# Optimization experiments

Hardware: AMD Instinct MI355X
Metric: run time of the kernel (lower is better)

The kernel has to match this reference:

```python
import jax, jax.numpy as jnp
import numpy as np

LEAKY_SLOPE = 0.2

def leaky_relu(x):
    return jnp.where(x >= 0, x, LEAKY_SLOPE * x)

def setup_inputs() -> dict:
    key = jax.random.key(0)
    ks = jax.random.split(key, 11)
    B, F = 512, 1024
    H1, H2, OUT = 512, 256, 128  # hidden_dims = [512, 256, 128]
    KD = 5                        # minibatch kernel dims
    x = jax.random.normal(ks[0], (B, F), dtype=jnp.float32)
    # features: Linear(F,H1) -> LReLU -> Linear(H1,H2) -> LReLU
    W1 = jax.random.normal(ks[1], (F, H1), dtype=jnp.float32) / np.sqrt(F)
    b1 = jnp.zeros((H1,), dtype=jnp.float32)
    W2 = jax.random.normal(ks[2], (H1, H2), dtype=jnp.float32) / np.sqrt(H1)
    b2 = jnp.zeros((H2,), dtype=jnp.float32)
    # minibatch discrimination tensor T: (in=H2, out=OUT, kernel=KD), N(0,1) init
    T = jax.random.normal(ks[3], (H2, OUT, KD), dtype=jnp.float32)
    # final: Linear(H2+OUT, OUT) -> LReLU -> Linear(OUT, 1)
    W3 = jax.random.normal(ks[4], (H2 + OUT, OUT), dtype=jnp.float32) / np.sqrt(H2 + OUT)
    b3 = jnp.zeros((OUT,), dtype=jnp.float32)
    W4 = jax.random.normal(ks[5], (OUT, 1), dtype=jnp.float32) / np.sqrt(OUT)
    b4 = jnp.zeros((1,), dtype=jnp.float32)
    return {"x": x, "W1": W1, "b1": b1, "W2": W2, "b2": b2,
            "T": T, "W3": W3, "b3": b3, "W4": W4, "b4": b4}

def reference(x, W1, b1, W2, b2, T, W3, b3, W4, b4):
    # MLP feature stack (dropout = identity in eval mode)
    h = leaky_relu(x @ W1 + b1)          # (B, 512)
    h = leaky_relu(h @ W2 + b2)          # (B, 256)
    # Minibatch discrimination
    in_f, out_f, kd = T.shape
    M = (h @ T.reshape(in_f, out_f * kd)).reshape(-1, out_f, kd)  # (B, out, kd)
    # pairwise L1 over kernel dim: (B, B, out)
    norm = jnp.abs(M[:, None, :, :] - M[None, :, :, :]).sum(-1)
    o_b = jnp.exp(-norm).sum(0) - 1.0    # (B, out); -1 removes self term
    z = jnp.concatenate([h, o_b], axis=1)  # (B, 256+128)
    z = leaky_relu(z @ W3 + b3)
    return z @ W4 + b4                    # (B, 1)
```

## Files before the change

### kernel.cpp

```cpp
#include <hip/hip_runtime.h>
#include <math.h>

#define B_   512
#define F_   1024
#define H1_  512
#define H2_  256
#define OUT_ 128
#define KD_  5
#define NT_  640
#define ZK_  384

typedef short bf16x8 __attribute__((ext_vector_type(8)));
typedef float f32x16 __attribute__((ext_vector_type(16)));

__device__ __forceinline__ float lrelu(float v) { return v >= 0.f ? v : 0.2f * v; }

__device__ __forceinline__ unsigned f2bf(float f) {
    unsigned u = __float_as_uint(f);
    return (u + 0x7fffu + ((u >> 16) & 1u)) >> 16;
}
__device__ __forceinline__ unsigned pack2bf(float a, float b) {
    return f2bf(a) | (f2bf(b) << 16);
}

#define NXB 256
#define NW1 512
#define NW2 128
#define NTT 160
#define PACK_BLOCKS (NXB + NW1 + NW2 + NTT + 48)

__global__ __launch_bounds__(256)
void pack_kernel(const float* __restrict__ x,  const float* __restrict__ W1,
                 const float* __restrict__ W2, const float* __restrict__ T,
                 const float* __restrict__ W3,
                 unsigned short* __restrict__ xb,  unsigned short* __restrict__ W1t,
                 unsigned short* __restrict__ W2t, unsigned short* __restrict__ Tt,
                 unsigned short* __restrict__ W3t)
{
    int b = blockIdx.x;
    const int t = threadIdx.x;
    if (b < NXB) {
        const int base = b * 2048 + t * 8;
        const float4 a = *(const float4*)(x + base);
        const float4 c = *(const float4*)(x + base + 4);
        uint4 o;
        o.x = pack2bf(a.x, a.y); o.y = pack2bf(a.z, a.w);
        o.z = pack2bf(c.x, c.y); o.w = pack2bf(c.z, c.w);
        *(uint4*)(xb + base) = o;
        return;
    }
    __shared__ float Tl[32][33];
    const float* src; unsigned short* dst; int R, C, tile;
    b -= NXB;
    if (b < NW1)              { src = W1; dst = W1t; R = 1024; C = 512; tile = b; }
    else if ((b -= NW1) < NW2){ src = W2; dst = W2t; R = 512;  C = 256; tile = b; }
    else if ((b -= NW2) < NTT){ src = T;  dst = Tt;  R = 256;  C = 640; tile = b; }
    else                      { b -= NTT;  src = W3; dst = W3t; R = 384; C = 128; tile = b; }
    const int tpc = C / 32;
    const int tr = tile / tpc, tc = tile % tpc;
    {
        const int col = t & 31, rr = t >> 5;
        #pragma unroll
        for (int p = 0; p < 4; ++p)
            Tl[rr + 8 * p][col] = src[(size_t)(tr * 32 + rr + 8 * p) * C + tc * 32 + col];
    }
    __syncthreads();
    const int orow = t >> 3, up = t & 7;
    unsigned* d = (unsigned*)(dst + (size_t)(tc * 32 + orow) * R + tr * 32);
    d[up]     = pack2bf(Tl[2 * up][orow],      Tl[2 * up + 1][orow]);
    d[up + 8] = pack2bf(Tl[2 * up + 16][orow], Tl[2 * up + 17][orow]);
}

template<int WAVES, int KSLICE, int LDA, int LDB,
         bool RELU, bool HAS_BIAS, bool BF16_OUT, bool CONCAT_A>
__global__ __launch_bounds__(WAVES * 64)
void gemm(const unsigned short* __restrict__ Ab,
          const float* __restrict__ obA, const float* __restrict__ obB,
          const unsigned short* __restrict__ Bt,
          const float* __restrict__ bias,
          void* __restrict__ Cout, int M, int N)
{
    __shared__ float Red[WAVES * 1024];
    const int tid  = threadIdx.x;
    const int wav  = tid >> 6;
    const int lane = tid & 63;
    const int half = lane >> 5;
    const int mn   = lane & 31;
    const int m0   = blockIdx.y * 32;
    const int n0   = blockIdx.x * 32;
    const int kw   = wav * KSLICE;

    f32x16 acc;
    #pragma unroll
    for (int i = 0; i < 16; ++i) acc[i] = 0.f;

    const unsigned short* arow = Ab + (size_t)(m0 + mn) * LDA;
    const unsigned short* brow = Bt + (size_t)(n0 + mn) * LDB;

    #pragma unroll
    for (int s = 0; s < KSLICE / 16; ++s) {
        const int k = kw + 16 * s + 8 * half;
        bf16x8 af, bf;
        if (CONCAT_A) {
            if (k < H2_) {
                af = *(const bf16x8*)&Ab[(size_t)(m0 + mn) * H2_ + k];
            } else {
                const float* pa = obA + (size_t)(m0 + mn) * OUT_ + (k - H2_);
                const float* pb = obB + (size_t)(m0 + mn) * OUT_ + (k - H2_);
                union { unsigned u[4]; bf16x8 v; } cv;
                #pragma unroll
                for (int jj = 0; jj < 4; ++jj)
                    cv.u[jj] = pack2bf(pa[2 * jj] + pb[2 * jj],
                                       pa[2 * jj + 1] + pb[2 * jj + 1]);
                af = cv.v;
            }
        } else {
            af = *(const bf16x8*)&arow[k];
        }
        bf = *(const bf16x8*)&brow[k];
        acc = __builtin_amdgcn_mfma_f32_32x32x16_bf16(af, bf, acc, 0, 0, 0);
    }

    #pragma unroll
    for (int r = 0; r < 16; ++r) {
        const int row = (r & 3) + 8 * (r >> 2) + 4 * half;
        Red[wav * 1024 + row * 32 + mn] = acc[r];
    }
    __syncthreads();

    if (tid < 256) {
        const int e0 = tid * 4, row = e0 >> 5, col = e0 & 31;
        float v[4];
        #pragma unroll
        for (int q = 0; q < 4; ++q) {
            float u = 0.f;
            #pragma unroll
            for (int w = 0; w < WAVES; ++w) u += Red[w * 1024 + e0 + q];
            if (HAS_BIAS) u += bias[n0 + col + q];
            if (RELU) u = lrelu(u);
            v[q] = u;
        }
        if (BF16_OUT) {
            uint2 o;
            o.x = pack2bf(v[0], v[1]); o.y = pack2bf(v[2], v[3]);
            *(uint2*)((unsigned short*)Cout + (size_t)(m0 + row) * N + n0 + col) = o;
        } else {
            *(float4*)((float*)Cout + (size_t)(m0 + row) * N + n0 + col) =
                make_float4(v[0], v[1], v[2], v[3]);
        }
    }
}

__global__ __launch_bounds__(128)
void disc_kernel(const float* __restrict__ Mt, float* __restrict__ obH)
{
    const int o  = blockIdx.x >> 3;
    const int jq = (blockIdx.x >> 1) & 3;
    const int ih = blockIdx.x & 1;
    const int t  = threadIdx.x;
    const int j  = jq * 128 + t;
    const int i0 = ih * 256;
    __shared__ float L[256 * 8];
    const float* base = Mt + (size_t)o * 5 * 512;
    #pragma unroll
    for (int k = 0; k < KD_; ++k) {
        L[t * 8 + k]         = base[k * 512 + i0 + t];
        L[(t + 128) * 8 + k] = base[k * 512 + i0 + t + 128];
    }
    const float mj0 = base[0 * 512 + j], mj1 = base[1 * 512 + j],
                mj2 = base[2 * 512 + j], mj3 = base[3 * 512 + j],
                mj4 = base[4 * 512 + j];
    __syncthreads();

    float acc0 = 0.f, acc1 = 0.f;
    #pragma unroll 4
    for (int i = 0; i < 256; i += 2) {
        {
            const float4 a = *(const float4*)&L[i * 8];
            const float n = fabsf(a.x - mj0) + fabsf(a.y - mj1) + fabsf(a.z - mj2)
                          + fabsf(a.w - mj3) + fabsf(L[i * 8 + 4] - mj4);
            acc0 += __expf(-n);
        }
        {
            const float4 a = *(const float4*)&L[(i + 1) * 8];
            const float n = fabsf(a.x - mj0) + fabsf(a.y - mj1) + fabsf(a.z - mj2)
                          + fabsf(a.w - mj3) + fabsf(L[(i + 1) * 8 + 4] - mj4);
            acc1 += __expf(-n);
        }
    }
    const float self = ((j >> 8) == ih) ? 1.f : 0.f;
    obH[(size_t)ih * B_ * OUT_ + (size_t)j * OUT_ + o] = acc0 + acc1 - self;
}

__global__ __launch_bounds__(256)
void final_dot(const float* __restrict__ z3, const float* __restrict__ W4,
               const float* __restrict__ b4, float* __restrict__ out)
{
    const int t = threadIdx.x;
    const int row = blockIdx.x * 64 + (t >> 2);
    const int q = t & 3;
    const float4* z = (const float4*)(z3 + (size_t)row * OUT_ + q * 32);
    const float4* w = (const float4*)(W4 + q * 32);
    float acc = 0.f;
    #pragma unroll
    for (int k = 0; k < 8; ++k) {
        const float4 a = z[k], b = w[k];
        acc += a.x * b.x + a.y * b.y + a.z * b.z + a.w * b.w;
    }
    acc += __shfl_down(acc, 2, 4);
    acc += __shfl_down(acc, 1, 4);
    if (q == 0) out[row] = acc + b4[0];
}

extern "C" void kernel_launch(void* const* d_in, const int* in_sizes, int n_in,
                              void* d_out, int out_size, void* d_ws, size_t ws_size,
                              hipStream_t stream) {
    const float* x  = (const float*)d_in[0];
    const float* W1 = (const float*)d_in[1];
    const float* b1 = (const float*)d_in[2];
    const float* W2 = (const float*)d_in[3];
    const float* b2 = (const float*)d_in[4];
    const float* T  = (const float*)d_in[5];
    const float* W3 = (const float*)d_in[6];
    const float* b3 = (const float*)d_in[7];
    const float* W4 = (const float*)d_in[8];
    const float* b4 = (const float*)d_in[9];
    float* out = (float*)d_out;

    char* ws = (char*)d_ws;
    float*          Mt  = (float*)(ws + 0);
    float*          obH = (float*)(ws + 1310720);
    float*          z3  = (float*)(ws + 1835008);
    unsigned short* xb  = (unsigned short*)(ws + 2097152);
    unsigned short* W1t = (unsigned short*)(ws + 3145728);
    unsigned short* W2t = (unsigned short*)(ws + 4194304);
    unsigned short* Tt  = (unsigned short*)(ws + 4456448);
    unsigned short* W3t = (unsigned short*)(ws + 4784128);
    unsigned short* h1b = (unsigned short*)(ws + 4882432);
    unsigned short* h2b = (unsigned short*)(ws + 5406720);

    pack_kernel<<<PACK_BLOCKS, 256, 0, stream>>>(x, W1, W2, T, W3,
                                                 xb, W1t, W2t, Tt, W3t);

    gemm<8, 128, F_, F_, true, true, true, false>
        <<<dim3(H1_ / 32, B_ / 32), 512, 0, stream>>>(
        xb, nullptr, nullptr, W1t, b1, h1b, B_, H1_);

    gemm<8, 64, H1_, H1_, true, true, true, false>
        <<<dim3(H2_ / 32, B_ / 32), 512, 0, stream>>>(
        h1b, nullptr, nullptr, W2t, b2, h2b, B_, H2_);

    gemm<4, 64, H2_, H2_, false, false, false, false>
        <<<dim3(B_ / 32, NT_ / 32), 256, 0, stream>>>(
        Tt, nullptr, nullptr, h2b, nullptr, Mt, NT_, B_);

    disc_kernel<<<1024, 128, 0, stream>>>(Mt, obH);

    gemm<8, 48, H2_, ZK_, true, true, false, true>
        <<<dim3(OUT_ / 32, B_ / 32), 512, 0, stream>>>(
        h2b, obH, obH + B_ * OUT_, W3t, b3, z3, B_, OUT_);

    final_dot<<<B_ / 64, 256, 0, stream>>>(z3, W4, b4, out);
}
```

Before: 114.2 us.

## Drop pack kernel by converting fp32 operands inline, fuse final GEMM with dot

```diff
diff --git a/kernel.cpp b/kernel.cpp
--- a/kernel.cpp
+++ b/kernel.cpp
@@ -23,62 +23,48 @@
     return f2bf(a) | (f2bf(b) << 16);
 }
 
-#define NXB 256
-#define NW1 512
-#define NW2 128
-#define NTT 160
-#define PACK_BLOCKS (NXB + NW1 + NW2 + NTT + 48)
-
-__global__ __launch_bounds__(256)
-void pack_kernel(const float* __restrict__ x,  const float* __restrict__ W1,
-                 const float* __restrict__ W2, const float* __restrict__ T,
-                 const float* __restrict__ W3,
-                 unsigned short* __restrict__ xb,  unsigned short* __restrict__ W1t,
-                 unsigned short* __restrict__ W2t, unsigned short* __restrict__ Tt,
-                 unsigned short* __restrict__ W3t)
-{
-    int b = blockIdx.x;
-    const int t = threadIdx.x;
-    if (b < NXB) {
-        const int base = b * 2048 + t * 8;
-        const float4 a = *(const float4*)(x + base);
-        const float4 c = *(const float4*)(x + base + 4);
-        uint4 o;
-        o.x = pack2bf(a.x, a.y); o.y = pack2bf(a.z, a.w);
-        o.z = pack2bf(c.x, c.y); o.w = pack2bf(c.z, c.w);
-        *(uint4*)(xb + base) = o;
-        return;
-    }
-    __shared__ float Tl[32][33];
-    const float* src; unsigned short* dst; int R, C, tile;
-    b -= NXB;
-    if (b < NW1)              { src = W1; dst = W1t; R = 1024; C = 512; tile = b; }
-    else if ((b -= NW1) < NW2){ src = W2; dst = W2t; R = 512;  C = 256; tile = b; }
-    else if ((b -= NW2) < NTT){ src = T;  dst = Tt;  R = 256;  C = 640; tile = b; }
-    else                      { b -= NTT;  src = W3; dst = W3t; R = 384; C = 128; tile = b; }
-    const int tpc = C / 32;
-    const int tr = tile / tpc, tc = tile % tpc;
-    {
-        const int col = t & 31, rr = t >> 5;
-        #pragma unroll
-        for (int p = 0; p < 4; ++p)
-            Tl[rr + 8 * p][col] = src[(size_t)(tr * 32 + rr + 8 * p) * C + tc * 32 + col];
-    }
-    __syncthreads();
-    const int orow = t >> 3, up = t & 7;
-    unsigned* d = (unsigned*)(dst + (size_t)(tc * 32 + orow) * R + tr * 32);
-    d[up]     = pack2bf(Tl[2 * up][orow],      Tl[2 * up + 1][orow]);
-    d[up + 8] = pack2bf(Tl[2 * up + 16][orow], Tl[2 * up + 17][orow]);
-}
-
-template<int WAVES, int KSLICE, int LDA, int LDB,
-         bool RELU, bool HAS_BIAS, bool BF16_OUT, bool CONCAT_A>
+__device__ __forceinline__ bf16x8 frag_bf16row(const unsigned short* p, int idx, int ld, int k) {
+    return *(const bf16x8*)(p + (size_t)idx * ld + k);
+}
+__device__ __forceinline__ bf16x8 frag_f32row(const float* p, int idx, int ld, int k) {
+    const float4 a = *(const float4*)(p + (size_t)idx * ld + k);
+    const float4 b = *(const float4*)(p + (size_t)idx * ld + k + 4);
+    union { unsigned u[4]; bf16x8 v; } cv;
+    cv.u[0] = pack2bf(a.x, a.y); cv.u[1] = pack2bf(a.z, a.w);
+    cv.u[2] = pack2bf(b.x, b.y); cv.u[3] = pack2bf(b.z, b.w);
+    return cv.v;
+}
+__device__ __forceinline__ bf16x8 frag_f32col(const float* p, int idx, int ld, int k) {
+    union { unsigned u[4]; bf16x8 v; } cv;
+    #pragma unroll
+    for (int jj = 0; jj < 4; ++jj)
+        cv.u[jj] = pack2bf(p[(size_t)(k + 2 * jj) * ld + idx],
+                           p[(size_t)(k + 2 * jj + 1) * ld + idx]);
+    return cv.v;
+}
+__device__ __forceinline__ bf16x8 frag_concat(const unsigned short* h2b,
+                                              const float* obA, const float* obB,
+                                              int idx, int k) {
+    if (k < H2_) return frag_bf16row(h2b, idx, H2_, k);
+    const float* pa = obA + (size_t)idx * OUT_ + (k - H2_);
+    const float* pb = obB + (size_t)idx * OUT_ + (k - H2_);
+    union { unsigned u[4]; bf16x8 v; } cv;
+    #pragma unroll
+    for (int jj = 0; jj < 4; ++jj)
+        cv.u[jj] = pack2bf(pa[2 * jj] + pb[2 * jj], pa[2 * jj + 1] + pb[2 * jj + 1]);
+    return cv.v;
+}
+
+#define M_BF16ROW 0
+#define M_F32ROW  1
+#define M_F32COL  2
+
+template<int WAVES, int KSLICE, int AMODE, int BMODE,
+         bool RELU, bool HAS_BIAS, bool BF16_OUT>
 __global__ __launch_bounds__(WAVES * 64)
-void gemm(const unsigned short* __restrict__ Ab,
-          const float* __restrict__ obA, const float* __restrict__ obB,
-          const unsigned short* __restrict__ Bt,
-          const float* __restrict__ bias,
-          void* __restrict__ Cout, int M, int N)
+void gemm_k(const void* __restrict__ Ap, const void* __restrict__ Bp,
+            const float* __restrict__ bias, void* __restrict__ Cout,
+            int M, int N, int LDA, int LDB)
 {
     __shared__ float Red[WAVES * 1024];
     const int tid  = threadIdx.x;
@@ -88,36 +74,20 @@
     const int mn   = lane & 31;
     const int m0   = blockIdx.y * 32;
     const int n0   = blockIdx.x * 32;
-    const int kw   = wav * KSLICE;
 
     f32x16 acc;
     #pragma unroll
     for (int i = 0; i < 16; ++i) acc[i] = 0.f;
 
-    const unsigned short* arow = Ab + (size_t)(m0 + mn) * LDA;
-    const unsigned short* brow = Bt + (size_t)(n0 + mn) * LDB;
-
     #pragma unroll
     for (int s = 0; s < KSLICE / 16; ++s) {
-        const int k = kw + 16 * s + 8 * half;
+        const int k = wav * KSLICE + 16 * s + 8 * half;
         bf16x8 af, bf;
-        if (CONCAT_A) {
-            if (k < H2_) {
-                af = *(const bf16x8*)&Ab[(size_t)(m0 + mn) * H2_ + k];
-            } else {
-                const float* pa = obA + (size_t)(m0 + mn) * OUT_ + (k - H2_);
-                const float* pb = obB + (size_t)(m0 + mn) * OUT_ + (k - H2_);
-                union { unsigned u[4]; bf16x8 v; } cv;
-                #pragma unroll
-                for (int jj = 0; jj < 4; ++jj)
-                    cv.u[jj] = pack2bf(pa[2 * jj] + pb[2 * jj],
-                                       pa[2 * jj + 1] + pb[2 * jj + 1]);
-                af = cv.v;
-            }
-        } else {
-            af = *(const bf16x8*)&arow[k];
-        }
-        bf = *(const bf16x8*)&brow[k];
+        if (AMODE == M_BF16ROW)      af = frag_bf16row((const unsigned short*)Ap, m0 + mn, LDA, k);
+        else if (AMODE == M_F32ROW)  af = frag_f32row((const float*)Ap, m0 + mn, LDA, k);
+        else                         af = frag_f32col((const float*)Ap, m0 + mn, LDA, k);
+        if (BMODE == M_BF16ROW)      bf = frag_bf16row((const unsigned short*)Bp, n0 + mn, LDB, k);
+        else                         bf = frag_f32col((const float*)Bp, n0 + mn, LDB, k);
         acc = __builtin_amdgcn_mfma_f32_32x32x16_bf16(af, bf, acc, 0, 0, 0);
     }
 
@@ -193,23 +163,53 @@
 }
 
 __global__ __launch_bounds__(256)
-void final_dot(const float* __restrict__ z3, const float* __restrict__ W4,
-               const float* __restrict__ b4, float* __restrict__ out)
+void gemm3_dot(const unsigned short* __restrict__ h2b,
+               const float* __restrict__ obA, const float* __restrict__ obB,
+               const float* __restrict__ W3, const float* __restrict__ b3,
+               const float* __restrict__ W4, const float* __restrict__ b4,
+               float* __restrict__ out)
 {
-    const int t = threadIdx.x;
-    const int row = blockIdx.x * 64 + (t >> 2);
-    const int q = t & 3;
-    const float4* z = (const float4*)(z3 + (size_t)row * OUT_ + q * 32);
-    const float4* w = (const float4*)(W4 + q * 32);
-    float acc = 0.f;
-    #pragma unroll
-    for (int k = 0; k < 8; ++k) {
-        const float4 a = z[k], b = w[k];
-        acc += a.x * b.x + a.y * b.y + a.z * b.z + a.w * b.w;
-    }
-    acc += __shfl_down(acc, 2, 4);
-    acc += __shfl_down(acc, 1, 4);
-    if (q == 0) out[row] = acc + b4[0];
+    __shared__ float Red[32 * 128];
+    const int tid  = threadIdx.x;
+    const int w    = tid >> 6;
+    const int lane = tid & 63;
+    const int half = lane >> 5;
+    const int mn   = lane & 31;
+    const int m0   = blockIdx.x * 32;
+    const int n0   = w * 32;
+
+    f32x16 acc;
+    #pragma unroll
+    for (int i = 0; i < 16; ++i) acc[i] = 0.f;
+
+    #pragma unroll
+    for (int s = 0; s < ZK_ / 16; ++s) {
+        const int k = 16 * s + 8 * half;
+        const bf16x8 af = frag_concat(h2b, obA, obB, m0 + mn, k);
+        const bf16x8 bf = frag_f32col(W3, n0 + mn, OUT_, k);
+        acc = __builtin_amdgcn_mfma_f32_32x32x16_bf16(af, bf, acc, 0, 0, 0);
+    }
+
+    #pragma unroll
+    for (int r = 0; r < 16; ++r) {
+        const int row = (r & 3) + 8 * (r >> 2) + 4 * half;
+        const int col = n0 + mn;
+        Red[row * 128 + col] = lrelu(acc[r] + b3[col]);
+    }
+    __syncthreads();
+
+    if (tid < 128) {
+        const int row = tid >> 2, q = tid & 3;
+        float a = 0.f;
+        #pragma unroll
+        for (int cc0 = 0; cc0 < 32; ++cc0) {
+            const int cc = (cc0 + tid) & 31;
+            a += Red[row * 128 + q * 32 + cc] * W4[q * 32 + cc];
+        }
+        a += __shfl_down(a, 2, 4);
+        a += __shfl_down(a, 1, 4);
+        if (q == 0) out[m0 + row] = a + b4[0];
+    }
 }
 
 extern "C" void kernel_launch(void* const* d_in, const int* in_sizes, int n_in,
@@ -230,35 +230,23 @@
     char* ws = (char*)d_ws;
     float*          Mt  = (float*)(ws + 0);
     float*          obH = (float*)(ws + 1310720);
-    float*          z3  = (float*)(ws + 1835008);
-    unsigned short* xb  = (unsigned short*)(ws + 2097152);
-    unsigned short* W1t = (unsigned short*)(ws + 3145728);
-    unsigned short* W2t = (unsigned short*)(ws + 4194304);
-    unsigned short* Tt  = (unsigned short*)(ws + 4456448);
-    unsigned short* W3t = (unsigned short*)(ws + 4784128);
-    unsigned short* h1b = (unsigned short*)(ws + 4882432);
-    unsigned short* h2b = (unsigned short*)(ws + 5406720);
-
-    pack_kernel<<<PACK_BLOCKS, 256, 0, stream>>>(x, W1, W2, T, W3,
-                                                 xb, W1t, W2t, Tt, W3t);
-
-    gemm<8, 128, F_, F_, true, true, true, false>
+    unsigned short* h1b = (unsigned short*)(ws + 1835008);
+    unsigned short* h2b = (unsigned short*)(ws + 2359296);
+
+    gemm_k<8, 128, M_F32ROW, M_F32COL, true, true, true>
         <<<dim3(H1_ / 32, B_ / 32), 512, 0, stream>>>(
-        xb, nullptr, nullptr, W1t, b1, h1b, B_, H1_);
-
-    gemm<8, 64, H1_, H1_, true, true, true, false>
+        x, W1, b1, h1b, B_, H1_, F_, H1_);
+
+    gemm_k<8, 64, M_BF16ROW, M_F32COL, true, true, true>
         <<<dim3(H2_ / 32, B_ / 32), 512, 0, stream>>>(
-        h1b, nullptr, nullptr, W2t, b2, h2b, B_, H2_);
-
-    gemm<4, 64, H2_, H2_, false, false, false, false>
+        h1b, W2, b2, h2b, B_, H2_, H1_, H2_);
+
+    gemm_k<4, 64, M_F32COL, M_BF16ROW, false, false, false>
         <<<dim3(B_ / 32, NT_ / 32), 256, 0, stream>>>(
-        Tt, nullptr, nullptr, h2b, nullptr, Mt, NT_, B_);
+        T, h2b, nullptr, Mt, NT_, B_, NT_, H2_);
 
     disc_kernel<<<1024, 128, 0, stream>>>(Mt, obH);
 
-    gemm<8, 48, H2_, ZK_, true, true, false, true>
-        <<<dim3(OUT_ / 32, B_ / 32), 512, 0, stream>>>(
-        h2b, obH, obH + B_ * OUT_, W3t, b3, z3, B_, OUT_);
-
-    final_dot<<<B_ / 64, 256, 0, stream>>>(z3, W4, b4, out);
-}
+    gemm3_dot<<<B_ / 32, 256, 0, stream>>>(
+        h2b, obH, obH + B_ * OUT_, W3, b3, W4, b4, out);
+}
```

Result: faster. 110.6 us (-3.1%).
